# Performance work log

Hardware: AMD Instinct MI355X
Metric: run time of the kernel (lower is better)

## Reference

```python
import jax, jax.numpy as jnp
import numpy as np

CORR = 5          # corr_size (patch_size)
UP = 2            # upsample_param
CH = [512, 1024, 512, 256, 256, 256]
SZ = [64, 32, 16, 8, 4, 2]   # pyramid spatial sizes; UP*2**i upsamples all to 128
B = 2
P = CORR * CORR

def upsample_nearest(x, f):
    # nn.Upsample(scale_factor=f, mode='nearest') for integer f
    return jnp.repeat(jnp.repeat(x, f, axis=2), f, axis=3)

def correlate(f1, f2):
    # spatial_correlation_sample: kernel=1, patch=CORR, stride=1, padding=0, dilation_patch=1
    # out[b, pi*CORR+pj, y, x] = sum_c f1[b,c,y,x] * f2[b,c,y+pi-r,x+pj-r] (zeros out of range)
    r = CORR // 2
    b, c, h, w = f1.shape
    f2p = jnp.pad(f2, ((0, 0), (0, 0), (r, r), (r, r)))
    outs = []
    for pi in range(CORR):
        for pj in range(CORR):
            sh = jax.lax.dynamic_slice(f2p, (0, 0, pi, pj), (b, c, h, w))
            outs.append(jnp.sum(f1 * sh, axis=1))
    return jnp.stack(outs, axis=1)  # [B, P, h, w]

def avgpool(x):
    # AvgPool2d(kernel_size=3, stride=2, padding=1), count_include_pad=True (torch default)
    s = jax.lax.reduce_window(x, 0.0, jax.lax.add, (1, 1, 3, 3), (1, 1, 2, 2), ((0, 0), (0, 0), (1, 1), (1, 1)))
    return s / 9.0

def conv3x3(x, w, b):
    y = jax.lax.conv_general_dilated(x, w, (1, 1), ((1, 1), (1, 1)), dimension_numbers=("NCHW", "OIHW", "NCHW"))
    return y + b[None, :, None, None]

def level_step(feat1, feat2, h_pre, c_pre, w, b, lvl):
    f = UP * (2 ** lvl)
    u1 = upsample_nearest(feat1, f)
    u2 = upsample_nearest(feat2, f)
    corr = jax.nn.leaky_relu(correlate(u1, u2), 0.01)
    # int(log2(up_W / feat_W)) pools; this is <= 6 so only avg_pooling1 is ever used
    for _ in range(int(np.log2(u1.shape[3] // feat1.shape[3]))):
        corr = avgpool(corr)
    gates = conv3x3(jnp.concatenate([corr, h_pre], axis=1), w, b)
    i = jax.nn.sigmoid(gates[:, :P])
    fg = jax.nn.sigmoid(gates[:, P:2 * P])
    o = jax.nn.sigmoid(gates[:, 2 * P:3 * P])
    g = jnp.tanh(gates[:, 3 * P:])
    c_next = fg * c_pre + i * g
    h_next = o * jnp.tanh(c_next)
    return h_next, c_next

def setup_inputs():
    keys = jax.random.split(jax.random.key(0), 40)
    d = {}
    k = 0
    for i in range(6):
        d[f"x{i}"] = jax.random.normal(keys[k], (B, CH[i], SZ[i], SZ[i]), jnp.float32); k += 1
        d[f"xp{i}"] = jax.random.normal(keys[k], (B, CH[i], SZ[i], SZ[i]), jnp.float32); k += 1
        d[f"h{i}"] = jax.random.normal(keys[k], (B, P, SZ[i], SZ[i]), jnp.float32); k += 1
        d[f"c{i}"] = jax.random.normal(keys[k], (B, P, SZ[i], SZ[i]), jnp.float32); k += 1
    for i in range(6):
        d[f"W{i}"] = jax.random.normal(keys[k], (4 * P, 2 * P, 3, 3), jnp.float32) * 0.05; k += 1
        d[f"b{i}"] = jnp.zeros((4 * P,), jnp.float32)
    return d

def reference(x0, x1, x2, x3, x4, x5, xp0, xp1, xp2, xp3, xp4, xp5,
              h0, h1, h2, h3, h4, h5, c0, c1, c2, c3, c4, c5,
              W0, W1, W2, W3, W4, W5, b0, b1, b2, b3, b4, b5):
    xs = [x0, x1, x2, x3, x4, x5]
    xps = [xp0, xp1, xp2, xp3, xp4, xp5]
    hs = [h0, h1, h2, h3, h4, h5]
    cs = [c0, c1, c2, c3, c4, c5]
    Ws = [W0, W1, W2, W3, W4, W5]
    bs = [b0, b1, b2, b3, b4, b5]
    outs = []
    for lvl in range(6):
        h_next, c_next = level_step(xs[lvl], xps[lvl], hs[lvl], cs[lvl], Ws[lvl], bs[lvl], lvl)
        outs.extend([h_next, c_next])
    return tuple(outs)
```

## Files before the change

kernel.cpp:

```cpp
#include <hip/hip_runtime.h>

#define NB 2
#define PP 25
#define NLVL 6

struct Params {
  const float* x1[NLVL];
  const float* x2[NLVL];
  const float* h[NLVL];
  const float* c[NLVL];
  const float* W[NLVL];
  const float* bias[NLVL];
  float* Dpart[NLVL];
  float* D[NLVL];
  float* pooled[NLVL];
  float* WT[NLVL];
  float* gates[NLVL];
  float* hout[NLVL];
  float* cout[NLVL];
};

__device__ __forceinline__ float lrelu(float v) { return v > 0.f ? v : 0.01f * v; }

__global__ __launch_bounds__(256) void repack_kernel(Params pr) {
  const int lvl = blockIdx.y;
  const float* W = pr.W[lvl];
  float* WT = pr.WT[lvl];
  for (int i = blockIdx.x * 256 + threadIdx.x; i < 100 * 450; i += gridDim.x * 256) {
    const int oc = i / 450;
    const int r = i - oc * 450;
    WT[r * 100 + oc] = W[i];
  }
}

__global__ __launch_bounds__(256) void dcorr_kernel(Params pr) {
  static const int SZt[6] = {64, 32, 16, 8, 4, 2};
  static const int CHt[6] = {512, 1024, 512, 256, 256, 256};
  static const int NCH[6] = {16, 16, 4, 1, 1, 1};
  static const int LGQ[6] = {4, 3, 2, 0, 0, 0};
  const int lvl = blockIdx.y;
  const int S = SZt[lvl], C = CHt[lvl], nch = NCH[lvl];
  const int rows = NB * S;
  const int bid = blockIdx.x;
  if (bid >= rows * nch) return;
  const int row = bid / nch;
  const int chunk = bid - row * nch;
  const int b = row / S, yb = row - b * S;
  const int tid = threadIdx.x;
  const size_t nlev = (size_t)NB * S * S * 9;
  float* part = pr.Dpart[lvl] + (size_t)chunk * nlev;

  __shared__ float red[9216];

  if (S >= 16) {
    const int lgq = LGQ[lvl];
    const int xqn = S >> 2;
    const int cgn = 256 >> lgq;
    const int xq = tid & (xqn - 1);
    const int cg = tid >> lgq;
    const int chpc = C / nch;
    const int cpt = chpc / cgn;
    const int xb0 = xq << 2;

    const float* f1b = pr.x1[lvl] + (size_t)b * C * S * S + (size_t)yb * S + xb0;
    const float* f2b = pr.x2[lvl] + (size_t)b * C * S * S;

    float acc[9][4];
#pragma unroll
    for (int jj = 0; jj < 9; ++jj)
#pragma unroll
      for (int j = 0; j < 4; ++j) acc[jj][j] = 0.f;

    const int c0 = chunk * chpc + cg;
    for (int t = 0; t < cpt; ++t) {
      const int cc = c0 + t * cgn;
      const float4 f1 = *(const float4*)(f1b + (size_t)cc * S * S);
      const float f1a[4] = {f1.x, f1.y, f1.z, f1.w};
      const float* p2 = f2b + (size_t)cc * S * S;
#pragma unroll
      for (int dy = 0; dy < 3; ++dy) {
        const int yy = yb + dy - 1;
        if (yy < 0 || yy >= S) continue;
        const float* prow = p2 + (size_t)yy * S;
        const float4 m = *(const float4*)(prow + xb0);
        const float lm = (xb0 > 0) ? prow[xb0 - 1] : 0.f;
        const float rm = (xb0 + 4 < S) ? prow[xb0 + 4] : 0.f;
        const float wl[4] = {lm, m.x, m.y, m.z};
        const float wc[4] = {m.x, m.y, m.z, m.w};
        const float wr[4] = {m.y, m.z, m.w, rm};
#pragma unroll
        for (int j = 0; j < 4; ++j) {
          acc[dy * 3 + 0][j] = fmaf(f1a[j], wl[j], acc[dy * 3 + 0][j]);
          acc[dy * 3 + 1][j] = fmaf(f1a[j], wc[j], acc[dy * 3 + 1][j]);
          acc[dy * 3 + 2][j] = fmaf(f1a[j], wr[j], acc[dy * 3 + 2][j]);
        }
      }
    }

    const int n = S * 9;
#pragma unroll
    for (int jj = 0; jj < 9; ++jj)
#pragma unroll
      for (int j = 0; j < 4; ++j)
        red[cg * n + (xb0 + j) * 9 + jj] = acc[jj][j];
    __syncthreads();
    for (int g = cgn >> 1; g >= 1; g >>= 1) {
      for (int i = tid; i < g * n; i += 256) {
        const int c = i / n, e = i - c * n;
        red[c * n + e] += red[(c + g) * n + e];
      }
      __syncthreads();
    }
    float* out = part + (size_t)(b * S + yb) * S * 9;
    for (int i = tid; i < n; i += 256) out[i] = red[i];
  } else {
    const int lg = (S == 8) ? 3 : ((S == 4) ? 2 : 1);
    const int xb = tid & (S - 1), cg = tid >> lg;
    const int NG = 256 >> lg;
    const int cpt = C / NG;

    const float* f1base = pr.x1[lvl] + (size_t)b * C * S * S + (size_t)yb * S + xb;
    const float* f2base = pr.x2[lvl] + (size_t)b * C * S * S;

    float acc[9];
#pragma unroll
    for (int j = 0; j < 9; ++j) acc[j] = 0.f;

    for (int t = 0; t < cpt; ++t) {
      const int cc = cg + t * NG;
      const float f1 = f1base[(size_t)cc * S * S];
      const float* p2 = f2base + (size_t)cc * S * S;
#pragma unroll
      for (int dy = 0; dy < 3; ++dy) {
        const int yy = yb + dy - 1;
        if (yy < 0 || yy >= S) continue;
        const float* prow = p2 + yy * S;
#pragma unroll
        for (int dx = 0; dx < 3; ++dx) {
          const int xx = xb + dx - 1;
          const float v = (xx >= 0 && xx < S) ? prow[xx] : 0.f;
          acc[dy * 3 + dx] += f1 * v;
        }
      }
    }

#pragma unroll
    for (int j = 0; j < 9; ++j) red[tid * 9 + j] = acc[j];
    __syncthreads();
    for (int g = NG >> 1; g >= 1; g >>= 1) {
      if (cg < g) {
#pragma unroll
        for (int j = 0; j < 9; ++j) red[tid * 9 + j] += red[(tid + g * S) * 9 + j];
      }
      __syncthreads();
    }
    if (cg == 0) {
      float* Dp = part + ((size_t)(b * S + yb) * S + xb) * 9;
#pragma unroll
      for (int j = 0; j < 9; ++j) Dp[j] = red[tid * 9 + j];
    }
  }
}

__global__ __launch_bounds__(256) void dreduce_kernel(Params pr) {
  static const int SZt[6] = {64, 32, 16, 8, 4, 2};
  static const int NCH[6] = {16, 16, 4, 1, 1, 1};
  const int lvl = blockIdx.y;
  const int S = SZt[lvl], nch = NCH[lvl];
  const int n = NB * S * S * 9;
  const int i = blockIdx.x * 256 + threadIdx.x;
  if (i >= n) return;
  const float* part = pr.Dpart[lvl];
  float s = 0.f;
  for (int c = 0; c < nch; ++c) s += part[(size_t)c * n + i];
  pr.D[lvl][i] = lrelu(s);
}

__global__ __launch_bounds__(256) void pool_kernel(Params pr) {
  static const int SZt[6] = {64, 32, 16, 8, 4, 2};
  static const int NYC[6] = {8, 4, 2, 1, 1, 1};
  static const int LGS[6] = {6, 5, 4, 3, 2, 1};
  const int lvl = blockIdx.y;
  const int S = SZt[lvl], k = lvl + 1, f = 1 << k, nyc = NYC[lvl], lgS = LGS[lvl];
  const int nyo = S / nyc;
  const int bid = blockIdx.x;
  if (bid >= 50 * nyc) return;
  const int yc = bid / 50;
  const int bp = bid - yc * 50;
  const int b = bp / 25, p = bp - (bp / 25) * 25;
  const int dpy = p / 5 - 2, dpx = p - (p / 5) * 5 - 2;
  const int tid = threadIdx.x;
  const int yo0 = yc * nyo;

  __shared__ float ckb[2][130], clb[2][66];
  __shared__ float Dl[5184];
  __shared__ float tmp[1024];

  if (tid == 0) { ckb[0][0] = 1.f; clb[0][0] = 1.f; }
  __syncthreads();
  int rj = 0, cur = 0;
  for (int j = 0; j < k; ++j) {
    const int half = 1 << j, rn = 2 * half - 1;
    float cknew = 0.f, clnew = 0.f;
    if (tid <= 2 * rn) {
      const int t = tid - rn;
#pragma unroll
      for (int e = -1; e <= 1; ++e) {
        const int u = t + e * half;
        if (u >= -rj && u <= rj) cknew += ckb[cur][u + rj];
      }
      cknew *= (1.f / 3.f);
    }
    if (tid < 2 * half) {
      const int y = tid;
      float s = (y < half) ? clb[cur][y] : 0.f;
      const int u = y - half;
      if (u >= -rj && u <= rj) s += ckb[cur][u + rj];
      clnew = s * (1.f / 3.f);
    }
    __syncthreads();
    if (tid <= 2 * rn) ckb[cur ^ 1][tid] = cknew;
    if (tid < 2 * half) clb[cur ^ 1][tid] = clnew;
    __syncthreads();
    cur ^= 1;
    rj = rn;
  }
  const float* ck = ckb[cur];
  const float* cl = clb[cur];

  const int yb0 = (yo0 > 0) ? yo0 - 1 : 0;
  const int nyb = (yo0 + nyo - 1) - yb0 + 1;
  const float* Dg = pr.D[lvl] + (size_t)b * S * S * 9 + (size_t)yb0 * S * 9;
  const int nload = nyb * S * 9;
  for (int i = tid; i < nload; i += 256) Dl[i] = Dg[i];
  __syncthreads();

  for (int item = tid; item < nyo * 128; item += 256) {
    const int yol = item >> 7, x = item & 127;
    const int yo = yo0 + yol;
    const int xb = x >> k, tx = x & (f - 1);
    const int txp = tx + dpx;
    const int dxi = (txp < 0) ? 0 : ((txp >= f) ? 2 : 1);
    float sum = 0.f;
    if (yo == 0) {
      for (int y = 0; y < f; ++y) {
        const int typ = y + dpy;
        const int dyi = (typ < 0) ? 0 : ((typ >= f) ? 2 : 1);
        sum += cl[y] * Dl[((0 - yb0) * S + xb) * 9 + dyi * 3 + dxi];
      }
    } else {
      const int ylo = yo * f - (f - 1);
      for (int t = 0; t < 2 * f - 1; ++t) {
        const int y = ylo + t;
        const int yb = y >> k, ty = y & (f - 1);
        const int typ = ty + dpy;
        const int dyi = (typ < 0) ? 0 : ((typ >= f) ? 2 : 1);
        sum += ck[t] * Dl[((yb - yb0) * S + xb) * 9 + dyi * 3 + dxi];
      }
    }
    tmp[yol * 128 + x] = sum;
  }
  __syncthreads();

  float* out = pr.pooled[lvl] + (size_t)(b * PP + p) * S * S;
  for (int item = tid; item < nyo * S; item += 256) {
    const int yol = item >> lgS, xo = item & (S - 1);
    float sum = 0.f;
    if (xo == 0) {
      for (int x = 0; x < f; ++x) sum += cl[x] * tmp[yol * 128 + x];
    } else {
      const int xlo = xo * f - (f - 1);
      for (int t = 0; t < 2 * f - 1; ++t) sum += ck[t] * tmp[yol * 128 + xlo + t];
    }
    out[(size_t)(yo0 + yol) * S + xo] = sum;
  }
}

__global__ __launch_bounds__(256) void conv_kernel(Params pr) {
  static const int SZt[6] = {64, 32, 16, 8, 4, 2};
  static const int LG[6]  = {6, 5, 4, 3, 2, 1};
  const int lvl = blockIdx.y;
  const int S = SZt[lvl], lg = LG[lvl];
  const int rows = NB * S;
  if ((int)blockIdx.x >= rows) return;
  const int b = blockIdx.x >> lg, y = blockIdx.x & (S - 1);
  const int q = blockIdx.z;
  const int tid = threadIdx.x;

  __shared__ float in_lds[3 * 50 * 68];
  const float* pooled = pr.pooled[lvl] + (size_t)b * PP * S * S;
  const float* hin = pr.h[lvl] + (size_t)b * PP * S * S;
  for (int i = tid; i < 150 * 68; i += 256) {
    const int r = i / 68, xi = i - r * 68;
    const int ky = r / 50, ic = r - ky * 50;
    const int yy = y + ky - 1;
    const int x = xi - 1;
    float v = 0.f;
    if (yy >= 0 && yy < S && x >= 0 && x < S)
      v = (ic < PP) ? pooled[((size_t)ic * S + yy) * S + x]
                    : hin[((size_t)(ic - PP) * S + yy) * S + x];
    in_lds[i] = v;
  }
  __syncthreads();

  const int nxc = (S >= 8) ? (S >> 3) : 1;
  const int nitems = PP * nxc;
  if (tid >= nitems) return;
  const int xs = tid / 25;
  const int p = tid - xs * 25;
  const int x0 = xs << 3;
  const int oc = q * PP + p;

  const float* WT = pr.WT[lvl];
  float acc[8];
#pragma unroll
  for (int xx = 0; xx < 8; ++xx) acc[xx] = 0.f;

  for (int ic = 0; ic < 50; ++ic) {
    const float* wrow = WT + (size_t)ic * 900 + oc;
#pragma unroll
    for (int ky = 0; ky < 3; ++ky) {
      const float w0 = wrow[(ky * 3 + 0) * 100];
      const float w1 = wrow[(ky * 3 + 1) * 100];
      const float w2 = wrow[(ky * 3 + 2) * 100];
      const float4* rp = (const float4*)&in_lds[(ky * 50 + ic) * 68];
      const int fi = x0 >> 2;
      const float4 A = rp[fi], Bv = rp[fi + 1], Cv = rp[fi + 2];
      const float sg[12] = {A.x, A.y, A.z, A.w, Bv.x, Bv.y, Bv.z, Bv.w,
                            Cv.x, Cv.y, Cv.z, Cv.w};
#pragma unroll
      for (int xx = 0; xx < 8; ++xx)
        acc[xx] = fmaf(w0, sg[xx], fmaf(w1, sg[xx + 1], fmaf(w2, sg[xx + 2], acc[xx])));
    }
  }

  const float bb = pr.bias[lvl][oc];
  float* g = pr.gates[lvl] + ((size_t)(q * NB + b) * PP + p) * S * S + (size_t)y * S + x0;
  if (S >= 8) {
    float4 o0, o1;
    o0.x = acc[0] + bb; o0.y = acc[1] + bb; o0.z = acc[2] + bb; o0.w = acc[3] + bb;
    o1.x = acc[4] + bb; o1.y = acc[5] + bb; o1.z = acc[6] + bb; o1.w = acc[7] + bb;
    ((float4*)g)[0] = o0;
    ((float4*)g)[1] = o1;
  } else {
#pragma unroll
    for (int xx = 0; xx < 8; ++xx)
      if (x0 + xx < S) g[xx] = acc[xx] + bb;
  }
}

__global__ __launch_bounds__(256) void lstm_kernel(Params pr) {
  static const int SZt[6] = {64, 32, 16, 8, 4, 2};
  const int lvl = blockIdx.y;
  const int S = SZt[lvl];
  const int n4 = (NB * PP * S * S) >> 2;
  const int i4 = blockIdx.x * 256 + threadIdx.x;
  if (i4 >= n4) return;
  const float4* g0 = (const float4*)pr.gates[lvl];
  const float4 vi = g0[i4];
  const float4 vf = g0[n4 + i4];
  const float4 vo = g0[2 * n4 + i4];
  const float4 vg = g0[3 * n4 + i4];
  const float4 vc = ((const float4*)pr.c[lvl])[i4];
  float4 hn, cn;
  const float* gi = (const float*)&vi;
  const float* gf = (const float*)&vf;
  const float* go = (const float*)&vo;
  const float* gg = (const float*)&vg;
  const float* cp = (const float*)&vc;
  float* hp = (float*)&hn;
  float* cq = (float*)&cn;
#pragma unroll
  for (int j = 0; j < 4; ++j) {
    const float i_ = 1.f / (1.f + __expf(-gi[j]));
    const float f_ = 1.f / (1.f + __expf(-gf[j]));
    const float o_ = 1.f / (1.f + __expf(-go[j]));
    const float g_ = 1.f - 2.f / (__expf(2.f * gg[j]) + 1.f);
    const float c_ = f_ * cp[j] + i_ * g_;
    const float t2 = 1.f - 2.f / (__expf(2.f * c_) + 1.f);
    cq[j] = c_;
    hp[j] = o_ * t2;
  }
  ((float4*)pr.hout[lvl])[i4] = hn;
  ((float4*)pr.cout[lvl])[i4] = cn;
}

extern "C" void kernel_launch(void* const* d_in, const int* in_sizes, int n_in,
                              void* d_out, int out_size, void* d_ws, size_t ws_size,
                              hipStream_t stream) {
  static const int SZ[NLVL] = {64, 32, 16, 8, 4, 2};
  static const int NCH[NLVL] = {16, 16, 4, 1, 1, 1};

  Params pr;
  float* ws = (float*)d_ws;
  size_t off = 0;
  for (int l = 0; l < NLVL; ++l) {
    pr.Dpart[l] = ws + off;
    off += (size_t)NCH[l] * NB * SZ[l] * SZ[l] * 9;
  }
  for (int l = 0; l < NLVL; ++l) { pr.D[l] = ws + off; off += (size_t)NB * SZ[l] * SZ[l] * 9; }
  for (int l = 0; l < NLVL; ++l) { pr.pooled[l] = ws + off; off += (size_t)NB * PP * SZ[l] * SZ[l]; }
  for (int l = 0; l < NLVL; ++l) { pr.WT[l] = ws + off; off += 100 * 450; }
  for (int l = 0; l < NLVL; ++l) { pr.gates[l] = ws + off; off += (size_t)4 * NB * PP * SZ[l] * SZ[l]; }

  float* out = (float*)d_out;
  size_t ooff = 0;
  for (int l = 0; l < NLVL; ++l) {
    pr.hout[l] = out + ooff; ooff += (size_t)NB * PP * SZ[l] * SZ[l];
    pr.cout[l] = out + ooff; ooff += (size_t)NB * PP * SZ[l] * SZ[l];
  }

  for (int l = 0; l < NLVL; ++l) {
    pr.x1[l] = (const float*)d_in[4 * l + 0];
    pr.x2[l] = (const float*)d_in[4 * l + 1];
    pr.h[l]  = (const float*)d_in[4 * l + 2];
    pr.c[l]  = (const float*)d_in[4 * l + 3];
    pr.W[l]    = (const float*)d_in[24 + 2 * l];
    pr.bias[l] = (const float*)d_in[25 + 2 * l];
  }

  repack_kernel<<<dim3(45, NLVL), 256, 0, stream>>>(pr);
  dcorr_kernel<<<dim3(2048, NLVL), 256, 0, stream>>>(pr);
  dreduce_kernel<<<dim3(288, NLVL), 256, 0, stream>>>(pr);
  pool_kernel<<<dim3(400, NLVL), 256, 0, stream>>>(pr);
  conv_kernel<<<dim3(128, NLVL, 4), 256, 0, stream>>>(pr);
  lstm_kernel<<<dim3(200, NLVL), 256, 0, stream>>>(pr);
}
```

Before: 274.3 us.

## Fuse LSTM gate activations into conv kernel and retile conv by x-tiles

Measured after the change: 308.7 us. 12.6% more time.

```diff
diff --git a/kernel.cpp b/kernel.cpp
--- a/kernel.cpp
+++ b/kernel.cpp
@@ -15,7 +15,6 @@
   float* D[NLVL];
   float* pooled[NLVL];
   float* WT[NLVL];
-  float* gates[NLVL];
   float* hout[NLVL];
   float* cout[NLVL];
 };
@@ -276,113 +275,140 @@
   }
 }
 
-__global__ __launch_bounds__(256) void conv_kernel(Params pr) {
+__global__ __launch_bounds__(128) void conv_kernel(Params pr) {
   static const int SZt[6] = {64, 32, 16, 8, 4, 2};
-  static const int LG[6]  = {6, 5, 4, 3, 2, 1};
+  static const int XTt[6] = {32, 32, 16, 8, 4, 2};
+  static const int NXGt[6] = {4, 4, 2, 1, 1, 1};
+  static const int WDt[6] = {36, 36, 20, 12, 12, 12};
   const int lvl = blockIdx.y;
-  const int S = SZt[lvl], lg = LG[lvl];
-  const int rows = NB * S;
-  if ((int)blockIdx.x >= rows) return;
-  const int b = blockIdx.x >> lg, y = blockIdx.x & (S - 1);
-  const int q = blockIdx.z;
+  const int S = SZt[lvl], xtile = XTt[lvl], nxg = NXGt[lvl], W = WDt[lvl];
+  const int nxt = S / xtile;
+  const int nblk = NB * S * nxt;
+  const int bid = blockIdx.x;
+  if (bid >= nblk) return;
+  const int b = bid / (S * nxt);
+  const int rem = bid - b * (S * nxt);
+  const int y = rem / nxt;
+  const int xt = rem - y * nxt;
+  const int xb0 = xt * xtile;
   const int tid = threadIdx.x;
 
-  __shared__ float in_lds[3 * 50 * 68];
+  __shared__ float in_lds[150 * 36];
   const float* pooled = pr.pooled[lvl] + (size_t)b * PP * S * S;
   const float* hin = pr.h[lvl] + (size_t)b * PP * S * S;
-  for (int i = tid; i < 150 * 68; i += 256) {
-    const int r = i / 68, xi = i - r * 68;
-    const int ky = r / 50, ic = r - ky * 50;
-    const int yy = y + ky - 1;
-    const int x = xi - 1;
-    float v = 0.f;
-    if (yy >= 0 && yy < S && x >= 0 && x < S)
-      v = (ic < PP) ? pooled[((size_t)ic * S + yy) * S + x]
-                    : hin[((size_t)(ic - PP) * S + yy) * S + x];
-    in_lds[i] = v;
+  {
+    const int tot = 150 * W;
+    int r = tid / W;
+    int j = tid - r * W;
+    for (int i = tid; i < tot; i += 128) {
+      const int ky = r / 50;
+      const int ic = r - ky * 50;
+      const int yy = y + ky - 1;
+      const int x = xb0 + j - 1;
+      float v = 0.f;
+      if (yy >= 0 && yy < S && x >= 0 && x < S)
+        v = (ic < PP) ? pooled[((size_t)ic * S + yy) * S + x]
+                      : hin[((size_t)(ic - PP) * S + yy) * S + x];
+      in_lds[r * W + j] = v;
+      j += 128;
+      while (j >= W) { j -= W; ++r; }
+    }
   }
   __syncthreads();
 
-  const int nxc = (S >= 8) ? (S >> 3) : 1;
-  const int nitems = PP * nxc;
-  if (tid >= nitems) return;
-  const int xs = tid / 25;
-  const int p = tid - xs * 25;
-  const int x0 = xs << 3;
-  const int oc = q * PP + p;
-
-  const float* WT = pr.WT[lvl];
-  float acc[8];
-#pragma unroll
-  for (int xx = 0; xx < 8; ++xx) acc[xx] = 0.f;
+  if (tid >= 25 * nxg) return;
+  const int xg = tid / 25;
+  const int p = tid - xg * 25;
+  const int xoff = xg * 8;
+
+  const float* wbase = pr.WT[lvl] + p;
+
+  float w[4][9], wn[4][9], acc[4][8];
+#pragma unroll
+  for (int q = 0; q < 4; ++q) {
+#pragma unroll
+    for (int t = 0; t < 9; ++t) w[q][t] = wbase[t * 100 + q * 25];
+#pragma unroll
+    for (int xx = 0; xx < 8; ++xx) acc[q][xx] = 0.f;
+  }
 
   for (int ic = 0; ic < 50; ++ic) {
-    const float* wrow = WT + (size_t)ic * 900 + oc;
+    const bool pre = (ic < 49);
+    if (pre) {
+      const float* wq = wbase + (size_t)(ic + 1) * 900;
+#pragma unroll
+      for (int q = 0; q < 4; ++q)
+#pragma unroll
+        for (int t = 0; t < 9; ++t) wn[q][t] = wq[t * 100 + q * 25];
+    }
 #pragma unroll
     for (int ky = 0; ky < 3; ++ky) {
-      const float w0 = wrow[(ky * 3 + 0) * 100];
-      const float w1 = wrow[(ky * 3 + 1) * 100];
-      const float w2 = wrow[(ky * 3 + 2) * 100];
-      const float4* rp = (const float4*)&in_lds[(ky * 50 + ic) * 68];
-      const int fi = x0 >> 2;
-      const float4 A = rp[fi], Bv = rp[fi + 1], Cv = rp[fi + 2];
+      const float4* rp = (const float4*)(in_lds + (ky * 50 + ic) * W);
+      const float4 A = rp[2 * xg];
+      const float4 Bv = rp[2 * xg + 1];
+      const float4 Cv = rp[2 * xg + 2];
       const float sg[12] = {A.x, A.y, A.z, A.w, Bv.x, Bv.y, Bv.z, Bv.w,
                             Cv.x, Cv.y, Cv.z, Cv.w};
 #pragma unroll
-      for (int xx = 0; xx < 8; ++xx)
-        acc[xx] = fmaf(w0, sg[xx], fmaf(w1, sg[xx + 1], fmaf(w2, sg[xx + 2], acc[xx])));
-    }
-  }
-
-  const float bb = pr.bias[lvl][oc];
-  float* g = pr.gates[lvl] + ((size_t)(q * NB + b) * PP + p) * S * S + (size_t)y * S + x0;
+      for (int q = 0; q < 4; ++q) {
+        const float w0 = w[q][ky * 3], w1 = w[q][ky * 3 + 1], w2 = w[q][ky * 3 + 2];
+#pragma unroll
+        for (int xx = 0; xx < 8; ++xx)
+          acc[q][xx] = fmaf(w0, sg[xx], fmaf(w1, sg[xx + 1], fmaf(w2, sg[xx + 2], acc[q][xx])));
+      }
+    }
+    if (pre) {
+#pragma unroll
+      for (int q = 0; q < 4; ++q)
+#pragma unroll
+        for (int t = 0; t < 9; ++t) w[q][t] = wn[q][t];
+    }
+  }
+
+  const float bi = pr.bias[lvl][p];
+  const float bf = pr.bias[lvl][p + 25];
+  const float bo = pr.bias[lvl][p + 50];
+  const float bg = pr.bias[lvl][p + 75];
+  const size_t base = ((size_t)(b * PP + p) * S + y) * S + xb0 + xoff;
+  const float* cin = pr.c[lvl] + base;
+  float* ho = pr.hout[lvl] + base;
+  float* co = pr.cout[lvl] + base;
+
+  float cp[8], hn[8], cn[8];
   if (S >= 8) {
-    float4 o0, o1;
-    o0.x = acc[0] + bb; o0.y = acc[1] + bb; o0.z = acc[2] + bb; o0.w = acc[3] + bb;
-    o1.x = acc[4] + bb; o1.y = acc[5] + bb; o1.z = acc[6] + bb; o1.w = acc[7] + bb;
-    ((float4*)g)[0] = o0;
-    ((float4*)g)[1] = o1;
+    const float4 c0 = ((const float4*)cin)[0];
+    const float4 c1 = ((const float4*)cin)[1];
+    cp[0] = c0.x; cp[1] = c0.y; cp[2] = c0.z; cp[3] = c0.w;
+    cp[4] = c1.x; cp[5] = c1.y; cp[6] = c1.z; cp[7] = c1.w;
   } else {
 #pragma unroll
+    for (int xx = 0; xx < 8; ++xx) cp[xx] = (xx < S) ? cin[xx] : 0.f;
+  }
+#pragma unroll
+  for (int xx = 0; xx < 8; ++xx) {
+    const float gi = acc[0][xx] + bi;
+    const float gf = acc[1][xx] + bf;
+    const float go = acc[2][xx] + bo;
+    const float gg = acc[3][xx] + bg;
+    const float i_ = 1.f / (1.f + __expf(-gi));
+    const float f_ = 1.f / (1.f + __expf(-gf));
+    const float o_ = 1.f / (1.f + __expf(-go));
+    const float g_ = 1.f - 2.f / (__expf(2.f * gg) + 1.f);
+    const float c_ = f_ * cp[xx] + i_ * g_;
+    const float t2 = 1.f - 2.f / (__expf(2.f * c_) + 1.f);
+    cn[xx] = c_;
+    hn[xx] = o_ * t2;
+  }
+  if (S >= 8) {
+    ((float4*)ho)[0] = make_float4(hn[0], hn[1], hn[2], hn[3]);
+    ((float4*)ho)[1] = make_float4(hn[4], hn[5], hn[6], hn[7]);
+    ((float4*)co)[0] = make_float4(cn[0], cn[1], cn[2], cn[3]);
+    ((float4*)co)[1] = make_float4(cn[4], cn[5], cn[6], cn[7]);
+  } else {
+#pragma unroll
     for (int xx = 0; xx < 8; ++xx)
-      if (x0 + xx < S) g[xx] = acc[xx] + bb;
-  }
-}
-
-__global__ __launch_bounds__(256) void lstm_kernel(Params pr) {
-  static const int SZt[6] = {64, 32, 16, 8, 4, 2};
-  const int lvl = blockIdx.y;
-  const int S = SZt[lvl];
-  const int n4 = (NB * PP * S * S) >> 2;
-  const int i4 = blockIdx.x * 256 + threadIdx.x;
-  if (i4 >= n4) return;
-  const float4* g0 = (const float4*)pr.gates[lvl];
-  const float4 vi = g0[i4];
-  const float4 vf = g0[n4 + i4];
-  const float4 vo = g0[2 * n4 + i4];
-  const float4 vg = g0[3 * n4 + i4];
-  const float4 vc = ((const float4*)pr.c[lvl])[i4];
-  float4 hn, cn;
-  const float* gi = (const float*)&vi;
-  const float* gf = (const float*)&vf;
-  const float* go = (const float*)&vo;
-  const float* gg = (const float*)&vg;
-  const float* cp = (const float*)&vc;
-  float* hp = (float*)&hn;
-  float* cq = (float*)&cn;
-#pragma unroll
-  for (int j = 0; j < 4; ++j) {
-    const float i_ = 1.f / (1.f + __expf(-gi[j]));
-    const float f_ = 1.f / (1.f + __expf(-gf[j]));
-    const float o_ = 1.f / (1.f + __expf(-go[j]));
-    const float g_ = 1.f - 2.f / (__expf(2.f * gg[j]) + 1.f);
-    const float c_ = f_ * cp[j] + i_ * g_;
-    const float t2 = 1.f - 2.f / (__expf(2.f * c_) + 1.f);
-    cq[j] = c_;
-    hp[j] = o_ * t2;
-  }
-  ((float4*)pr.hout[lvl])[i4] = hn;
-  ((float4*)pr.cout[lvl])[i4] = cn;
+      if (xx < S) { ho[xx] = hn[xx]; co[xx] = cn[xx]; }
+  }
 }
 
 extern "C" void kernel_launch(void* const* d_in, const int* in_sizes, int n_in,
@@ -401,7 +427,6 @@
   for (int l = 0; l < NLVL; ++l) { pr.D[l] = ws + off; off += (size_t)NB * SZ[l] * SZ[l] * 9; }
   for (int l = 0; l < NLVL; ++l) { pr.pooled[l] = ws + off; off += (size_t)NB * PP * SZ[l] * SZ[l]; }
   for (int l = 0; l < NLVL; ++l) { pr.WT[l] = ws + off; off += 100 * 450; }
-  for (int l = 0; l < NLVL; ++l) { pr.gates[l] = ws + off; off += (size_t)4 * NB * PP * SZ[l] * SZ[l]; }
 
   float* out = (float*)d_out;
   size_t ooff = 0;
@@ -423,6 +448,5 @@
   dcorr_kernel<<<dim3(2048, NLVL), 256, 0, stream>>>(pr);
   dreduce_kernel<<<dim3(288, NLVL), 256, 0, stream>>>(pr);
   pool_kernel<<<dim3(400, NLVL), 256, 0, stream>>>(pr);
-  conv_kernel<<<dim3(128, NLVL, 4), 256, 0, stream>>>(pr);
-  lstm_kernel<<<dim3(200, NLVL), 256, 0, stream>>>(pr);
-}
+  conv_kernel<<<dim3(256, NLVL), 128, 0, stream>>>(pr);
+}
```
